# Kernel tuning notes

Measured on AMD Instinct MI355X. Metric: run time of the kernel, lower is better.

## Reference

```python
import jax, jax.numpy as jnp
import numpy as np

N_NODES = 100000
N_EDGES = 1600000
IN_CH = 16
HID = 128
N_LAYERS = 4
OUT_CH = 3


def setup_inputs() -> dict:
    key = jax.random.key(0)
    ks = jax.random.split(key, 8)
    x = jax.random.normal(ks[0], (N_NODES, IN_CH), dtype=jnp.float32)
    edge_index = jax.random.randint(ks[1], (2, N_EDGES), 0, N_NODES, dtype=jnp.int64)
    # glorot-ish scaled params
    enc_W = jax.random.normal(ks[2], (IN_CH, HID), dtype=jnp.float32) * (1.0 / np.sqrt(IN_CH))
    enc_b = jnp.zeros((HID,), dtype=jnp.float32)
    conv_W = jax.random.normal(ks[3], (N_LAYERS, HID, HID), dtype=jnp.float32) * (1.0 / np.sqrt(HID))
    conv_b = jnp.zeros((N_LAYERS, HID), dtype=jnp.float32)
    dec_W = jax.random.normal(ks[4], (HID, OUT_CH), dtype=jnp.float32) * (1.0 / np.sqrt(HID))
    dec_b = jnp.zeros((OUT_CH,), dtype=jnp.float32)
    return {"x": x, "edge_index": edge_index, "enc_W": enc_W, "enc_b": enc_b,
            "conv_W": conv_W, "conv_b": conv_b, "dec_W": dec_W, "dec_b": dec_b}


def _gcn_forward(x, edge_index, enc_W, enc_b, conv_W, conv_b, dec_W, dec_b):
    n = x.shape[0]
    # PyG GCNConv: add self-loops, symmetric deg^-1/2 normalization
    loops = jnp.arange(n, dtype=edge_index.dtype)
    src = jnp.concatenate([edge_index[0], loops])  # [E+N]
    dst = jnp.concatenate([edge_index[1], loops])  # [E+N]
    deg = jax.ops.segment_sum(jnp.ones_like(dst, dtype=x.dtype), dst, num_segments=n)
    dinv = jnp.where(deg > 0, jax.lax.rsqrt(deg), 0.0)
    norm = (dinv[src] * dinv[dst])[:, None]  # [E+N, 1]

    h = jax.nn.relu(x @ enc_W + enc_b)  # encoder + ReLU
    for l in range(conv_W.shape[0]):
        hw = h @ conv_W[l]                      # [N, H] transform
        msg = hw[src] * norm                    # gather + normalize
        h = jax.ops.segment_sum(msg, dst, num_segments=n) + conv_b[l]
        h = jax.nn.relu(h)
    return h @ dec_W + dec_b  # decoder [N, 3]


def reference(x, edge_index, enc_W, enc_b, conv_W, conv_b, dec_W, dec_b):
    return _gcn_forward(x, edge_index, enc_W, enc_b, conv_W, conv_b, dec_W, dec_b)
```

## Files before the change

### kernel.cpp

```cpp
#include <hip/hip_runtime.h>


typedef float f32x4 __attribute__((ext_vector_type(4)));
typedef _Float16 h8 __attribute__((ext_vector_type(8)));

#define BKT_CAP 6144


__global__ __launch_bounds__(256) void k_bin(const int* __restrict__ src, const int* __restrict__ dst,
                                             int* __restrict__ bcnt, unsigned* __restrict__ ebuf, int E, int NB) {
  __shared__ int hist[512];
  __shared__ int lofs[512];
  int tid = threadIdx.x;
  int base = blockIdx.x * 4096;
  for (int i = tid; i < NB; i += 256) hist[i] = 0;
  __syncthreads();
  unsigned rec[16];
  int bk[16];
#pragma unroll
  for (int j = 0; j < 16; j++) {
    int e = base + j * 256 + tid;
    bk[j] = -1;
    if (e < E) {
      int d = dst[e];
      rec[j] = ((unsigned)(d & 255) << 24) | (unsigned)src[e];
      bk[j] = d >> 8;
      atomicAdd(&hist[bk[j]], 1);
    }
  }
  __syncthreads();
  for (int i = tid; i < NB; i += 256) {
    int c = hist[i];
    lofs[i] = c ? atomicAdd(&bcnt[i], c) : 0;
    hist[i] = 0;
  }
  __syncthreads();
#pragma unroll
  for (int j = 0; j < 16; j++) {
    if (bk[j] >= 0) {
      int p = lofs[bk[j]] + atomicAdd(&hist[bk[j]], 1);
      if (p < BKT_CAP) ebuf[(size_t)bk[j] * BKT_CAP + p] = rec[j];
    }
  }
}

__global__ __launch_bounds__(512) void k_bscan(const int* __restrict__ bcnt, int* __restrict__ bbase,
                                               int* __restrict__ rp, int NB, int N, int E) {
  __shared__ int wsum[8];
  int tid = threadIdx.x;
  int v = (tid < NB) ? bcnt[tid] : 0;
  int l = tid & 63, w = tid >> 6;
  int s = v;
#pragma unroll
  for (int off = 1; off < 64; off <<= 1) { int t = __shfl_up(s, off); if (l >= off) s += t; }
  if (l == 63) wsum[w] = s;
  __syncthreads();
  int woff = 0;
  for (int i = 0; i < w; i++) woff += wsum[i];
  if (tid < NB) bbase[tid] = woff + s - v;
  if (tid == 0) rp[N] = E;
}

__global__ __launch_bounds__(256) void k_bfill(const unsigned* __restrict__ ebuf, const int* __restrict__ bcnt,
                                               const int* __restrict__ bbase, int* __restrict__ rp,
                                               float* __restrict__ dinv, int* __restrict__ col, int N) {
  __shared__ int h[256];
  __shared__ int wsum[4];
  int b = blockIdx.x, tid = threadIdx.x;
  h[tid] = 0;
  __syncthreads();
  int n = min(bcnt[b], BKT_CAP);
  int bb = bbase[b];
  const unsigned* eb = ebuf + (size_t)b * BKT_CAP;
  for (int i = tid; i < n; i += 256) atomicAdd(&h[eb[i] >> 24], 1);
  __syncthreads();
  int cntv = h[tid];
  int l = tid & 63, wv = tid >> 6;
  int s = cntv;
#pragma unroll
  for (int off = 1; off < 64; off <<= 1) { int t = __shfl_up(s, off); if (l >= off) s += t; }
  if (l == 63) wsum[wv] = s;
  __syncthreads();
  int woff = 0;
  for (int i = 0; i < wv; i++) woff += wsum[i];
  int lpre = woff + s - cntv;
  int d = (b << 8) + tid;
  if (d < N) {
    rp[d] = bb + lpre;
    dinv[d] = 1.0f / sqrtf((float)(cntv + 1));
  }
  __syncthreads();
  h[tid] = lpre;
  __syncthreads();
  for (int i = tid; i < n; i += 256) {
    unsigned r = eb[i];
    int dlow = r >> 24;
    int pos = bb + atomicAdd(&h[dlow], 1);
    col[pos] = (int)(r & 0xFFFFFFu);
  }
}

__global__ __launch_bounds__(128) void k_prep_w(const float* __restrict__ convW, _Float16* __restrict__ Whi,
                                                _Float16* __restrict__ Wlo) {
  int lk = blockIdx.x;
  int l = lk >> 7, k = lk & 127, c = threadIdx.x;
  float x = convW[((size_t)l * 128 + k) * 128 + c];
  _Float16 hi = (_Float16)x;
  _Float16 lo = (_Float16)((x - (float)hi) * 2048.0f);
  size_t o = ((size_t)l * 128 + c) * 128 + k;
  Whi[o] = hi;
  Wlo[o] = lo;
}

__global__ __launch_bounds__(256) void k_encoder(const float* __restrict__ x, const float* __restrict__ W,
                                                 const float* __restrict__ b, const float* __restrict__ dinv,
                                                 _Float16* __restrict__ Hp, int N) {
  int node = blockIdx.x * 2 + (threadIdx.x >> 7);
  int c = threadIdx.x & 127;
  if (node >= N) return;
  const float* xr = x + (size_t)node * 16;
  float acc = b[c];
#pragma unroll
  for (int k = 0; k < 16; k++) acc = fmaf(xr[k], W[k * 128 + c], acc);
  Hp[(size_t)node * 128 + c] = (_Float16)(dinv[node] * fmaxf(acc, 0.0f));
}

__global__ __launch_bounds__(512, 4) void k_layer(const _Float16* __restrict__ Hp, const int* __restrict__ rp,
                                                  const int* __restrict__ col, const float* __restrict__ dinv,
                                                  const _Float16* __restrict__ Whi, const _Float16* __restrict__ Wlo,
                                                  const float* __restrict__ bias, _Float16* __restrict__ Hn,
                                                  const float* __restrict__ decW, const float* __restrict__ decb,
                                                  float* __restrict__ out, int last, int N) {
  __shared__ __align__(16) ushort ldsM[128 * 128];
  __shared__ __align__(16) ushort ldsW[128 * 64];
  char* mB = reinterpret_cast<char*>(ldsM);
  char* wB = reinterpret_cast<char*>(ldsW);
  const int tid = threadIdx.x;
  const int row0 = blockIdx.x * 128;

  {
    int grp = tid >> 4, ln = tid & 15;
#pragma unroll
    for (int t = 0; t < 4; t++) {
      int lrow = grp * 4 + t;
      int d = row0 + lrow;
      int moff = (lrow * 256 + ln * 16) ^ ((lrow & 7) << 4);
      h8 z = {(_Float16)0, (_Float16)0, (_Float16)0, (_Float16)0,
              (_Float16)0, (_Float16)0, (_Float16)0, (_Float16)0};
      if (d < N) {
        h8 a0 = z, a1 = z, a2 = z, a3 = z;
        a0 += *reinterpret_cast<const h8*>(Hp + (size_t)d * 128 + ln * 8);
        int e0 = rp[d], e1 = rp[d + 1];
        int i = e0;
        for (; i + 3 < e1; i += 4) {
          int s0 = col[i], s1 = col[i + 1], s2 = col[i + 2], s3 = col[i + 3];
          a0 += *reinterpret_cast<const h8*>(Hp + (size_t)s0 * 128 + ln * 8);
          a1 += *reinterpret_cast<const h8*>(Hp + (size_t)s1 * 128 + ln * 8);
          a2 += *reinterpret_cast<const h8*>(Hp + (size_t)s2 * 128 + ln * 8);
          a3 += *reinterpret_cast<const h8*>(Hp + (size_t)s3 * 128 + ln * 8);
        }
        if (i < e1)     a1 += *reinterpret_cast<const h8*>(Hp + (size_t)col[i] * 128 + ln * 8);
        if (i + 1 < e1) a2 += *reinterpret_cast<const h8*>(Hp + (size_t)col[i + 1] * 128 + ln * 8);
        if (i + 2 < e1) a3 += *reinterpret_cast<const h8*>(Hp + (size_t)col[i + 2] * 128 + ln * 8);
        h8 m;
#pragma unroll
        for (int j = 0; j < 8; j++) {
          float f = ((float)a0[j] + (float)a1[j]) + ((float)a2[j] + (float)a3[j]);
          m[j] = (_Float16)f;
        }
        *reinterpret_cast<h8*>(mB + moff) = m;
      } else {
        *reinterpret_cast<h8*>(mB + moff) = z;
      }
    }
  }
  __syncthreads();

  const int w = tid >> 6, l = tid & 63;
  const int wm = w >> 1, wn = w & 1;
  const int lr = l & 15, lg = l >> 4;
  f32x4 zero4 = {0.0f, 0.0f, 0.0f, 0.0f};
  f32x4 acc[2][4], acc2[2][4];
#pragma unroll
  for (int m = 0; m < 2; m++)
#pragma unroll
    for (int n = 0; n < 4; n++) { acc[m][n] = zero4; acc2[m][n] = zero4; }

  for (int half = 0; half < 2; half++) {
#pragma unroll
    for (int plane = 0; plane < 2; plane++) {
      if (half | plane) __syncthreads();
      const _Float16* Wp = plane ? Wlo : Whi;
#pragma unroll
      for (int i = 0; i < 2; i++) {
        int g = tid + i * 512;
        int c = g >> 3, c16 = g & 7;
        uint4 v = *reinterpret_cast<const uint4*>(Wp + (size_t)c * 128 + half * 64 + c16 * 8);
        *reinterpret_cast<uint4*>(wB + ((c * 128 + c16 * 16) ^ ((c & 7) << 4))) = v;
      }
      __syncthreads();
#pragma unroll
      for (int ksl = 0; ksl < 2; ksl++) {
        int kb = (ksl * 32 + lg * 8) * 2;
        h8 ah[2];
#pragma unroll
        for (int m = 0; m < 2; m++) {
          int row = wm * 32 + m * 16 + lr;
          ah[m] = *reinterpret_cast<const h8*>(mB + ((row * 256 + half * 128 + kb) ^ ((row & 7) << 4)));
        }
        h8 wf[4];
#pragma unroll
        for (int n = 0; n < 4; n++) {
          int colr = wn * 64 + n * 16 + lr;
          wf[n] = *reinterpret_cast<const h8*>(wB + ((colr * 128 + kb) ^ ((colr & 7) << 4)));
        }
        if (plane == 0) {
#pragma unroll
          for (int m = 0; m < 2; m++)
#pragma unroll
            for (int n = 0; n < 4; n++)
              acc[m][n] = __builtin_amdgcn_mfma_f32_16x16x32_f16(ah[m], wf[n], acc[m][n], 0, 0, 0);
        } else {
#pragma unroll
          for (int m = 0; m < 2; m++)
#pragma unroll
            for (int n = 0; n < 4; n++)
              acc2[m][n] = __builtin_amdgcn_mfma_f32_16x16x32_f16(ah[m], wf[n], acc2[m][n], 0, 0, 0);
        }
      }
    }
  }

  if (last) __syncthreads();
#pragma unroll
  for (int m = 0; m < 2; m++) {
    int lbase = wm * 32 + m * 16 + lg * 4;
#pragma unroll
    for (int r = 0; r < 4; r++) {
      int lrow = lbase + r;
      int grow = row0 + lrow;
      if (grow < N) {
        float dv = dinv[grow];
#pragma unroll
        for (int n = 0; n < 4; n++) {
          int colc = wn * 64 + n * 16 + lr;
          float val = acc[m][n][r] + 4.8828125e-4f * acc2[m][n][r];
          float h = fmaxf(fmaf(dv, val, bias[colc]), 0.0f);
          if (!last) {
            Hn[(size_t)grow * 128 + colc] = (_Float16)(dv * h);
          } else {
            _Float16 hf = (_Float16)h;
            *reinterpret_cast<ushort*>(mB + ((lrow * 256 + colc * 2) ^ ((lrow & 7) << 4))) =
                *reinterpret_cast<ushort*>(&hf);
          }
        }
      }
    }
  }

  if (last) {
    __syncthreads();
    int grp = tid >> 4, ln = tid & 15;
#pragma unroll
    for (int t = 0; t < 4; t++) {
      int lrow = grp * 4 + t;
      int d = row0 + lrow;
      if (d < N) {
        h8 hv = *reinterpret_cast<const h8*>(mB + ((lrow * 256 + ln * 16) ^ ((lrow & 7) << 4)));
        float p0 = 0.f, p1 = 0.f, p2 = 0.f;
#pragma unroll
        for (int j = 0; j < 8; j++) {
          int c = ln * 8 + j;
          float o = (float)hv[j];
          p0 = fmaf(o, decW[c * 3 + 0], p0);
          p1 = fmaf(o, decW[c * 3 + 1], p1);
          p2 = fmaf(o, decW[c * 3 + 2], p2);
        }
#pragma unroll
        for (int off = 8; off > 0; off >>= 1) {
          p0 += __shfl_xor(p0, off);
          p1 += __shfl_xor(p1, off);
          p2 += __shfl_xor(p2, off);
        }
        if (ln == 0) {
          out[(size_t)d * 3 + 0] = p0 + decb[0];
          out[(size_t)d * 3 + 1] = p1 + decb[1];
          out[(size_t)d * 3 + 2] = p2 + decb[2];
        }
      }
    }
  }
}

extern "C" void kernel_launch(void* const* d_in, const int* in_sizes, int n_in,
                              void* d_out, int out_size, void* d_ws, size_t ws_size,
                              hipStream_t stream) {
  const float* x     = (const float*)d_in[0];
  const int*   ei    = (const int*)d_in[1];
  const float* encW  = (const float*)d_in[2];
  const float* encb  = (const float*)d_in[3];
  const float* convW = (const float*)d_in[4];
  const float* convb = (const float*)d_in[5];
  const float* decW  = (const float*)d_in[6];
  const float* decb  = (const float*)d_in[7];
  const int N = in_sizes[0] / 16;
  const int E = in_sizes[1] / 2;
  const int L = in_sizes[4] / (128 * 128);
  const int* src = ei;
  const int* dst = ei + E;
  const int NB = (N + 255) >> 8;

  char* p = (char*)d_ws;
  auto alloc = [&](size_t bytes) -> void* {
    void* q = (void*)p;
    p += (bytes + 255) & ~(size_t)255;
    return q;
  };
  int*       rp     = (int*)alloc((size_t)(N + 1) * 4);
  int*       bcnt   = (int*)alloc((size_t)NB * 4);
  int*       bbase  = (int*)alloc((size_t)NB * 4);
  float*     dinv   = (float*)alloc((size_t)N * 4);
  int*       colA   = (int*)alloc((size_t)E * 4);
  _Float16*  HA     = (_Float16*)alloc((size_t)N * 128 * 2);
  size_t hb_bytes   = (size_t)N * 128 * 2;
  size_t ebuf_bytes = (size_t)NB * BKT_CAP * 4;
  void*  hb_union   = alloc(hb_bytes > ebuf_bytes ? hb_bytes : ebuf_bytes);
  _Float16* HB      = (_Float16*)hb_union;
  unsigned* ebuf    = (unsigned*)hb_union;
  _Float16*  Whi    = (_Float16*)alloc((size_t)L * 128 * 128 * 2);
  _Float16*  Wlo    = (_Float16*)alloc((size_t)L * 128 * 128 * 2);

  hipMemsetAsync(bcnt, 0, (size_t)NB * 4, stream);
  k_bin<<<(E + 4095) / 4096, 256, 0, stream>>>(src, dst, bcnt, ebuf, E, NB);
  k_bscan<<<1, 512, 0, stream>>>(bcnt, bbase, rp, NB, N, E);
  k_bfill<<<NB, 256, 0, stream>>>(ebuf, bcnt, bbase, rp, dinv, colA, N);
  k_prep_w<<<L * 128, 128, 0, stream>>>(convW, Whi, Wlo);
  k_encoder<<<(N + 1) / 2, 256, 0, stream>>>(x, encW, encb, dinv, HA, N);
  int gblocks = (N + 127) / 128;
  _Float16* Hp = HA;
  _Float16* Hn = HB;
  for (int l = 0; l < L; l++) {
    int last = (l == L - 1) ? 1 : 0;
    k_layer<<<gblocks, 512, 0, stream>>>(Hp, rp, colA, dinv, Whi + (size_t)l * 128 * 128,
                                         Wlo + (size_t)l * 128 * 128, convb + l * 128, Hn,
                                         decW, decb, (float*)d_out, last, N);
    _Float16* t = Hp; Hp = Hn; Hn = t;
  }
}
```

Before: 531.1 us.

## Read split-fp16 weights directly from global and merge hi/lo accumulators

Drops the shared-memory staging of the hi/lo fp16 weight planes in the layer kernel; each wave loads its weight fragments straight from global memory and the barriers around staging go away. The lo plane is no longer scaled by 2048, so hi and lo MFMAs accumulate into a single accumulator set, halving accumulator registers. With the 16 KB weight LDS buffer gone, launch bounds are raised to allow more blocks per CU to hide gather latency. Risks are extra global/L2 traffic for weights and reduced precision of the unscaled fp16 residual (possible subnormal flushing).

```diff
diff --git a/kernel.cpp b/kernel.cpp
--- a/kernel.cpp
+++ b/kernel.cpp
@@ -106,7 +106,7 @@
   int l = lk >> 7, k = lk & 127, c = threadIdx.x;
   float x = convW[((size_t)l * 128 + k) * 128 + c];
   _Float16 hi = (_Float16)x;
-  _Float16 lo = (_Float16)((x - (float)hi) * 2048.0f);
+  _Float16 lo = (_Float16)(x - (float)hi);
   size_t o = ((size_t)l * 128 + c) * 128 + k;
   Whi[o] = hi;
   Wlo[o] = lo;
@@ -125,16 +125,14 @@
   Hp[(size_t)node * 128 + c] = (_Float16)(dinv[node] * fmaxf(acc, 0.0f));
 }
 
-__global__ __launch_bounds__(512, 4) void k_layer(const _Float16* __restrict__ Hp, const int* __restrict__ rp,
+__global__ __launch_bounds__(512, 6) void k_layer(const _Float16* __restrict__ Hp, const int* __restrict__ rp,
                                                   const int* __restrict__ col, const float* __restrict__ dinv,
                                                   const _Float16* __restrict__ Whi, const _Float16* __restrict__ Wlo,
                                                   const float* __restrict__ bias, _Float16* __restrict__ Hn,
                                                   const float* __restrict__ decW, const float* __restrict__ decb,
                                                   float* __restrict__ out, int last, int N) {
   __shared__ __align__(16) ushort ldsM[128 * 128];
-  __shared__ __align__(16) ushort ldsW[128 * 64];
   char* mB = reinterpret_cast<char*>(ldsM);
-  char* wB = reinterpret_cast<char*>(ldsW);
   const int tid = threadIdx.x;
   const int row0 = blockIdx.x * 128;
 
@@ -180,53 +178,34 @@
   const int wm = w >> 1, wn = w & 1;
   const int lr = l & 15, lg = l >> 4;
   f32x4 zero4 = {0.0f, 0.0f, 0.0f, 0.0f};
-  f32x4 acc[2][4], acc2[2][4];
+  f32x4 acc[2][4];
 #pragma unroll
   for (int m = 0; m < 2; m++)
 #pragma unroll
-    for (int n = 0; n < 4; n++) { acc[m][n] = zero4; acc2[m][n] = zero4; }
-
+    for (int n = 0; n < 4; n++) acc[m][n] = zero4;
+
+#pragma unroll
   for (int half = 0; half < 2; half++) {
 #pragma unroll
-    for (int plane = 0; plane < 2; plane++) {
-      if (half | plane) __syncthreads();
-      const _Float16* Wp = plane ? Wlo : Whi;
-#pragma unroll
-      for (int i = 0; i < 2; i++) {
-        int g = tid + i * 512;
-        int c = g >> 3, c16 = g & 7;
-        uint4 v = *reinterpret_cast<const uint4*>(Wp + (size_t)c * 128 + half * 64 + c16 * 8);
-        *reinterpret_cast<uint4*>(wB + ((c * 128 + c16 * 16) ^ ((c & 7) << 4))) = v;
-      }
-      __syncthreads();
-#pragma unroll
-      for (int ksl = 0; ksl < 2; ksl++) {
-        int kb = (ksl * 32 + lg * 8) * 2;
-        h8 ah[2];
-#pragma unroll
-        for (int m = 0; m < 2; m++) {
-          int row = wm * 32 + m * 16 + lr;
-          ah[m] = *reinterpret_cast<const h8*>(mB + ((row * 256 + half * 128 + kb) ^ ((row & 7) << 4)));
-        }
-        h8 wf[4];
-#pragma unroll
-        for (int n = 0; n < 4; n++) {
-          int colr = wn * 64 + n * 16 + lr;
-          wf[n] = *reinterpret_cast<const h8*>(wB + ((colr * 128 + kb) ^ ((colr & 7) << 4)));
-        }
-        if (plane == 0) {
-#pragma unroll
-          for (int m = 0; m < 2; m++)
-#pragma unroll
-            for (int n = 0; n < 4; n++)
-              acc[m][n] = __builtin_amdgcn_mfma_f32_16x16x32_f16(ah[m], wf[n], acc[m][n], 0, 0, 0);
-        } else {
-#pragma unroll
-          for (int m = 0; m < 2; m++)
-#pragma unroll
-            for (int n = 0; n < 4; n++)
-              acc2[m][n] = __builtin_amdgcn_mfma_f32_16x16x32_f16(ah[m], wf[n], acc2[m][n], 0, 0, 0);
-        }
+    for (int ksl = 0; ksl < 2; ksl++) {
+      int ko = half * 64 + ksl * 32 + lg * 8;
+      h8 ah[2];
+#pragma unroll
+      for (int m = 0; m < 2; m++) {
+        int row = wm * 32 + m * 16 + lr;
+        ah[m] = *reinterpret_cast<const h8*>(mB + ((row * 256 + ko * 2) ^ ((row & 7) << 4)));
+      }
+#pragma unroll
+      for (int n = 0; n < 4; n++) {
+        int colr = wn * 64 + n * 16 + lr;
+        h8 wh = *reinterpret_cast<const h8*>(Whi + (size_t)colr * 128 + ko);
+        h8 wl = *reinterpret_cast<const h8*>(Wlo + (size_t)colr * 128 + ko);
+#pragma unroll
+        for (int m = 0; m < 2; m++)
+          acc[m][n] = __builtin_amdgcn_mfma_f32_16x16x32_f16(ah[m], wh, acc[m][n], 0, 0, 0);
+#pragma unroll
+        for (int m = 0; m < 2; m++)
+          acc[m][n] = __builtin_amdgcn_mfma_f32_16x16x32_f16(ah[m], wl, acc[m][n], 0, 0, 0);
       }
     }
   }
@@ -244,8 +223,7 @@
 #pragma unroll
         for (int n = 0; n < 4; n++) {
           int colc = wn * 64 + n * 16 + lr;
-          float val = acc[m][n][r] + 4.8828125e-4f * acc2[m][n][r];
-          float h = fmaxf(fmaf(dv, val, bias[colc]), 0.0f);
+          float h = fmaxf(fmaf(dv, acc[m][n][r], bias[colc]), 0.0f);
           if (!last) {
             Hn[(size_t)grow * 128 + colc] = (_Float16)(dv * h);
           } else {
```

Measured after the change: 657.3 us. 23.8% more time.
